# Kernel optimization log

Measured on AMD Instinct MI355X. Metric: run time of the kernel, lower is better.

The kernel has to match this reference:

```python
import jax, jax.numpy as jnp
import numpy as np

DIM = 256          # args.dim
MAX_Z = 100        # args.max_z
N_ATOM_EMBED = DIM - 1  # Euclidean manifold: dim - 1
B, N = 256, 128    # graphs, nodes per graph
E = B * N * N      # fully connected edges per batch, flattened
NORM_CONSTANT = 1.0


def setup_inputs() -> dict:
    key = jax.random.key(0)
    ks = jax.random.split(key, 8)
    x = jax.random.normal(ks[0], (B, N, 3), dtype=jnp.float32)
    categories = jax.random.randint(ks[1], (B, N), 0, MAX_Z)
    charges = jax.random.normal(ks[2], (B, N, 1), dtype=jnp.float32)
    edges = jax.random.randint(ks[3], (2, E), 0, B * N)
    node_mask = jnp.ones((B, N, 1), dtype=jnp.float32)
    edge_mask = jnp.ones((E, 1), dtype=jnp.float32)
    # nn.Embedding(max_z, n_atom_embed, padding_idx=0): row 0 is zeros
    emb = jax.random.normal(ks[4], (MAX_Z, N_ATOM_EMBED), dtype=jnp.float32)
    emb_table = emb.at[0].set(0.0)
    # nn.Linear(dim, 2*dim)
    lim = 1.0 / np.sqrt(DIM)
    W = jax.random.uniform(ks[5], (DIM, 2 * DIM), minval=-lim, maxval=lim, dtype=jnp.float32)
    b_lin = jax.random.uniform(ks[6], (2 * DIM,), minval=-lim, maxval=lim, dtype=jnp.float32)
    return {"x": x, "categories": categories, "charges": charges, "edges": edges,
            "node_mask": node_mask, "edge_mask": edge_mask,
            "emb_table": emb_table, "W": W, "b_lin": b_lin}


def coord2diff(x, edges, norm_constant=NORM_CONSTANT):
    row, col = edges[0], edges[1]
    coord_diff = x[row] - x[col]                              # [E, 3] gather + diff
    radial = jnp.sum(coord_diff * coord_diff, axis=1, keepdims=True)  # [E, 1]
    norm = jnp.sqrt(radial + 1e-8)
    coord_diff = coord_diff / (norm + norm_constant)
    return radial, coord_diff


def reference(x, categories, charges, edges, node_mask, edge_mask, emb_table, W, b_lin):
    h = emb_table[categories]                      # [B, N, dim-1] embedding lookup
    h = jnp.concatenate([charges, h], axis=2)      # [B, N, dim]
    b, n_nodes, d = h.shape
    xf = x.reshape(b * n_nodes, 3)
    nm = node_mask.reshape(b * n_nodes, 1)
    h = h.reshape(b * n_nodes, d) * nm             # masked node features
    radial, coord_diff = coord2diff(xf, edges)     # edge-index gather + norm
    # encode() pass-through (abstract layers treated as identity), then head
    parameters = h @ W + b_lin                     # [B*N, 2*dim] mean/logvar
    return parameters, radial, coord_diff
```

## Files before the change

### kernel.cpp

```cpp
#include <hip/hip_runtime.h>

typedef unsigned short u16;
typedef unsigned int u32;
typedef __attribute__((ext_vector_type(8))) short bf16x8;
typedef __attribute__((ext_vector_type(4))) float f32x4;

#define DIM 256
#define NOUT 512
#define MROWS 32768
#define NNODE 32768
#define NEDGE (256*128*128)
#define PARAM_SZ (32768*512)

__device__ __forceinline__ u16 f2bf(float f) {
    u32 x = __float_as_uint(f);
    u32 r = (x + 0x7FFFu + ((x >> 16) & 1u)) >> 16;
    return (u16)r;
}
__device__ __forceinline__ float bf2f(u16 u) {
    union { u32 i; float f; } v; v.i = ((u32)u) << 16; return v.f;
}

__global__ __launch_bounds__(1024) void transpose_kernel(const float* __restrict__ W,
                                                         u16* __restrict__ Wt) {
    __shared__ u16 tile[32][33];
    int n0 = blockIdx.x * 32;
    int k0 = blockIdx.y * 32;
    int tx = threadIdx.x, ty = threadIdx.y;
    tile[ty][tx] = f2bf(W[(k0 + ty) * NOUT + n0 + tx]);
    __syncthreads();
    Wt[(n0 + ty) * DIM + k0 + tx] = tile[tx][ty];
}

__global__ __launch_bounds__(256) void pack_kernel(const float* __restrict__ x,
                                                   const float* __restrict__ emb,
                                                   float4* __restrict__ xp,
                                                   u16* __restrict__ embp) {
    int i = blockIdx.x * 256 + threadIdx.x;
    if (i < NNODE) {
        float4 v;
        v.x = x[i * 3 + 0]; v.y = x[i * 3 + 1]; v.z = x[i * 3 + 2]; v.w = 0.0f;
        xp[i] = v;
    }
    if (i < 100 * 256) {
        int col = i & 255;
        int row = i >> 8;
        embp[i] = (col == 0) ? (u16)0 : f2bf(emb[row * 255 + col - 1]);
    }
}

__global__ __launch_bounds__(256) void edge_kernel(const int* __restrict__ edges,
                                                   const float4* __restrict__ xp,
                                                   float* __restrict__ radial_out,
                                                   float* __restrict__ cd_out) {
    __shared__ float buf[3072];
    const int tid = threadIdx.x;
    const int t4 = blockIdx.x * 256 + tid;
    int4 r4 = ((const int4*)edges)[t4];
    int4 c4 = ((const int4*)(edges + NEDGE))[t4];

    float4 xr0 = xp[r4.x], xr1 = xp[r4.y], xr2 = xp[r4.z], xr3 = xp[r4.w];
    float4 xc0 = xp[c4.x], xc1 = xp[c4.y], xc2 = xp[c4.z], xc3 = xp[c4.w];

    float4 rad;
    float cdv[12];
    #pragma unroll
    for (int e = 0; e < 4; ++e) {
        float4 a = (e == 0) ? xr0 : (e == 1) ? xr1 : (e == 2) ? xr2 : xr3;
        float4 b = (e == 0) ? xc0 : (e == 1) ? xc1 : (e == 2) ? xc2 : xc3;
        float dx = a.x - b.x, dy = a.y - b.y, dz = a.z - b.z;
        float r = dx * dx + dy * dy + dz * dz;
        float inv = 1.0f / (sqrtf(r + 1e-8f) + 1.0f);
        ((float*)&rad)[e] = r;
        cdv[e * 3 + 0] = dx * inv;
        cdv[e * 3 + 1] = dy * inv;
        cdv[e * 3 + 2] = dz * inv;
    }
    ((float4*)radial_out)[t4] = rad;

    #pragma unroll
    for (int k = 0; k < 3; ++k)
        ((float4*)buf)[tid * 3 + k] = ((const float4*)cdv)[k];
    __syncthreads();
    float4* cdg = (float4*)(cd_out + (size_t)blockIdx.x * 3072);
    #pragma unroll
    for (int k = 0; k < 3; ++k)
        cdg[k * 256 + tid] = ((const float4*)buf)[k * 256 + tid];
}

__global__ __launch_bounds__(256, 2) void gemm_kernel(const int* __restrict__ cats,
                                                      const float* __restrict__ charges,
                                                      const float* __restrict__ nmask,
                                                      const u16* __restrict__ embp,
                                                      const u16* __restrict__ Wt,
                                                      const float* __restrict__ bias,
                                                      float* __restrict__ out) {
    __shared__ u16 h_lds[64][DIM + 8];
    const int m0 = blockIdx.x * 64;
    const int tid = threadIdx.x;

    {
        int r = tid >> 2;
        int q = tid & 3;
        int m = m0 + r;
        float mask = nmask[m];
        const uint4* src = (const uint4*)(embp + (size_t)cats[m] * 256 + q * 64);
        uint4 v[8];
        #pragma unroll
        for (int t = 0; t < 8; ++t) v[t] = src[t];
        if (mask != 1.0f) {
            #pragma unroll
            for (int t = 0; t < 8; ++t) {
                u32* w = (u32*)&v[t];
                #pragma unroll
                for (int j = 0; j < 4; ++j) {
                    u16 lo = f2bf(bf2f((u16)(w[j] & 0xFFFF)) * mask);
                    u16 hi = f2bf(bf2f((u16)(w[j] >> 16)) * mask);
                    w[j] = (u32)lo | ((u32)hi << 16);
                }
            }
        }
        if (q == 0) {
            u32* w0 = (u32*)&v[0];
            w0[0] = (w0[0] & 0xFFFF0000u) | (u32)f2bf(charges[m] * mask);
        }
        #pragma unroll
        for (int t = 0; t < 8; ++t)
            *(uint4*)&h_lds[r][q * 64 + t * 8] = v[t];
    }
    __syncthreads();

    const int wave = tid >> 6;
    const int lane = tid & 63;
    const int lrow = lane & 15;
    const int quad = lane >> 4;
    const int nbase = wave * 128;

    f32x4 acc[4][8];
    #pragma unroll
    for (int ms = 0; ms < 4; ++ms)
        #pragma unroll
        for (int nt = 0; nt < 8; ++nt) acc[ms][nt] = (f32x4)(0.0f);

    #pragma unroll
    for (int k0 = 0; k0 < DIM; k0 += 32) {
        bf16x8 a[4];
        #pragma unroll
        for (int ms = 0; ms < 4; ++ms)
            a[ms] = *(const bf16x8*)&h_lds[ms * 16 + lrow][k0 + quad * 8];
        #pragma unroll
        for (int nt = 0; nt < 8; ++nt) {
            bf16x8 bfr = *(const bf16x8*)&Wt[(size_t)(nbase + nt * 16 + lrow) * DIM + k0 + quad * 8];
            #pragma unroll
            for (int ms = 0; ms < 4; ++ms)
                acc[ms][nt] = __builtin_amdgcn_mfma_f32_16x16x32_bf16(a[ms], bfr, acc[ms][nt], 0, 0, 0);
        }
    }

    #pragma unroll
    for (int nt = 0; nt < 8; ++nt) {
        int n = nbase + nt * 16 + lrow;
        float bv = bias[n];
        #pragma unroll
        for (int ms = 0; ms < 4; ++ms)
            #pragma unroll
            for (int r = 0; r < 4; ++r)
                out[(size_t)(m0 + ms * 16 + quad * 4 + r) * NOUT + n] = acc[ms][nt][r] + bv;
    }
}

extern "C" void kernel_launch(void* const* d_in, const int* in_sizes, int n_in,
                              void* d_out, int out_size, void* d_ws, size_t ws_size,
                              hipStream_t stream) {
    const float* x       = (const float*)d_in[0];
    const int*   cats    = (const int*)d_in[1];
    const float* charges = (const float*)d_in[2];
    const int*   edges   = (const int*)d_in[3];
    const float* nmask   = (const float*)d_in[4];
    const float* emb     = (const float*)d_in[6];
    const float* W       = (const float*)d_in[7];
    const float* bias    = (const float*)d_in[8];

    float* out    = (float*)d_out;
    float* params = out;
    float* radial = out + PARAM_SZ;
    float* cd     = out + PARAM_SZ + NEDGE;

    u16*    Wt   = (u16*)d_ws;
    float4* xp   = (float4*)((char*)d_ws + 256 * 1024);
    u16*    embp = (u16*)((char*)d_ws + 768 * 1024);

    transpose_kernel<<<dim3(16, 8), dim3(32, 32), 0, stream>>>(W, Wt);
    pack_kernel<<<NNODE / 256, 256, 0, stream>>>(x, emb, xp, embp);
    edge_kernel<<<NEDGE / 1024, 256, 0, stream>>>(edges, xp, radial, cd);
    gemm_kernel<<<MROWS / 64, 256, 0, stream>>>(cats, charges, nmask, embp, Wt, bias, params);
}
```

Measured before the change: 242.3 us.

## Merge prep kernels and co-schedule GEMM with edge work in one launch

Folds the weight transpose, coordinate packing and embedding packing into one prep kernel, cutting launches from four to two. The edge and GEMM kernels become one grid where the first 512 blocks do the GEMM and the remaining blocks do edges, so compute-bound and memory-bound work can share the GPU. In exchange, edge blocks now get the larger shared-memory footprint and the 256,2 launch bounds of the GEMM, which may lower their occupancy.

```diff
diff --git a/kernel.cpp b/kernel.cpp
--- a/kernel.cpp
+++ b/kernel.cpp
@@ -11,6 +11,8 @@
 #define NNODE 32768
 #define NEDGE (256*128*128)
 #define PARAM_SZ (32768*512)
+#define GEMM_BLOCKS 512
+#define EDGE_BLOCKS 4096
 
 __device__ __forceinline__ u16 f2bf(float f) {
     u32 x = __float_as_uint(f);
@@ -21,41 +23,51 @@
     union { u32 i; float f; } v; v.i = ((u32)u) << 16; return v.f;
 }
 
-__global__ __launch_bounds__(1024) void transpose_kernel(const float* __restrict__ W,
-                                                         u16* __restrict__ Wt) {
-    __shared__ u16 tile[32][33];
-    int n0 = blockIdx.x * 32;
-    int k0 = blockIdx.y * 32;
-    int tx = threadIdx.x, ty = threadIdx.y;
-    tile[ty][tx] = f2bf(W[(k0 + ty) * NOUT + n0 + tx]);
-    __syncthreads();
-    Wt[(n0 + ty) * DIM + k0 + tx] = tile[tx][ty];
-}
-
-__global__ __launch_bounds__(256) void pack_kernel(const float* __restrict__ x,
+__global__ __launch_bounds__(256) void prep_kernel(const float* __restrict__ W,
+                                                   const float* __restrict__ x,
                                                    const float* __restrict__ emb,
+                                                   u16* __restrict__ Wt,
                                                    float4* __restrict__ xp,
                                                    u16* __restrict__ embp) {
-    int i = blockIdx.x * 256 + threadIdx.x;
-    if (i < NNODE) {
+    const int b = blockIdx.x;
+    const int tid = threadIdx.x;
+    if (b < 128) {
+        __shared__ u16 tile[32][33];
+        int k0 = (b >> 4) * 32;
+        int n0 = (b & 15) * 32;
+        int tx = tid & 31, ty0 = tid >> 5;
+        #pragma unroll
+        for (int j = 0; j < 4; ++j) {
+            int ty = ty0 + j * 8;
+            tile[ty][tx] = f2bf(W[(k0 + ty) * NOUT + n0 + tx]);
+        }
+        __syncthreads();
+        #pragma unroll
+        for (int j = 0; j < 4; ++j) {
+            int ty = ty0 + j * 8;
+            Wt[(n0 + ty) * DIM + k0 + tx] = tile[tx][ty];
+        }
+    } else if (b < 256) {
+        int i = (b - 128) * 256 + tid;
         float4 v;
         v.x = x[i * 3 + 0]; v.y = x[i * 3 + 1]; v.z = x[i * 3 + 2]; v.w = 0.0f;
         xp[i] = v;
-    }
-    if (i < 100 * 256) {
+    } else {
+        int i = (b - 256) * 256 + tid;
         int col = i & 255;
         int row = i >> 8;
         embp[i] = (col == 0) ? (u16)0 : f2bf(emb[row * 255 + col - 1]);
     }
 }
 
-__global__ __launch_bounds__(256) void edge_kernel(const int* __restrict__ edges,
-                                                   const float4* __restrict__ xp,
-                                                   float* __restrict__ radial_out,
-                                                   float* __restrict__ cd_out) {
-    __shared__ float buf[3072];
-    const int tid = threadIdx.x;
-    const int t4 = blockIdx.x * 256 + tid;
+
+__device__ __forceinline__ void edge_part(int eb, int tid,
+                                          const int* __restrict__ edges,
+                                          const float4* __restrict__ xp,
+                                          float* __restrict__ radial_out,
+                                          float* __restrict__ cd_out,
+                                          float* buf ) {
+    const int t4 = eb * 256 + tid;
     int4 r4 = ((const int4*)edges)[t4];
     int4 c4 = ((const int4*)(edges + NEDGE))[t4];
 
@@ -82,22 +94,22 @@
     for (int k = 0; k < 3; ++k)
         ((float4*)buf)[tid * 3 + k] = ((const float4*)cdv)[k];
     __syncthreads();
-    float4* cdg = (float4*)(cd_out + (size_t)blockIdx.x * 3072);
+    float4* cdg = (float4*)(cd_out + (size_t)eb * 3072);
     #pragma unroll
     for (int k = 0; k < 3; ++k)
         cdg[k * 256 + tid] = ((const float4*)buf)[k * 256 + tid];
 }
 
-__global__ __launch_bounds__(256, 2) void gemm_kernel(const int* __restrict__ cats,
-                                                      const float* __restrict__ charges,
-                                                      const float* __restrict__ nmask,
-                                                      const u16* __restrict__ embp,
-                                                      const u16* __restrict__ Wt,
-                                                      const float* __restrict__ bias,
-                                                      float* __restrict__ out) {
-    __shared__ u16 h_lds[64][DIM + 8];
-    const int m0 = blockIdx.x * 64;
-    const int tid = threadIdx.x;
+__device__ __forceinline__ void gemm_part(int gb, int tid,
+                                          const int* __restrict__ cats,
+                                          const float* __restrict__ charges,
+                                          const float* __restrict__ nmask,
+                                          const u16* __restrict__ embp,
+                                          const u16* __restrict__ Wt,
+                                          const float* __restrict__ bias,
+                                          float* __restrict__ out,
+                                          u16 (*h_lds)[DIM + 8]) {
+    const int m0 = gb * 64;
 
     {
         int r = tid >> 2;
@@ -169,6 +181,26 @@
     }
 }
 
+__global__ __launch_bounds__(256, 2) void main_kernel(const int* __restrict__ cats,
+                                                      const float* __restrict__ charges,
+                                                      const float* __restrict__ nmask,
+                                                      const u16* __restrict__ embp,
+                                                      const u16* __restrict__ Wt,
+                                                      const float* __restrict__ bias,
+                                                      const int* __restrict__ edges,
+                                                      const float4* __restrict__ xp,
+                                                      float* __restrict__ params,
+                                                      float* __restrict__ radial,
+                                                      float* __restrict__ cd) {
+    __shared__ char smem[64 * (DIM + 8) * sizeof(u16)];
+    if (blockIdx.x < GEMM_BLOCKS)
+        gemm_part(blockIdx.x, threadIdx.x, cats, charges, nmask, embp, Wt, bias, params,
+                  (u16 (*)[DIM + 8])smem);
+    else
+        edge_part(blockIdx.x - GEMM_BLOCKS, threadIdx.x, edges, xp, radial, cd,
+                  (float*)smem);
+}
+
 extern "C" void kernel_launch(void* const* d_in, const int* in_sizes, int n_in,
                               void* d_out, int out_size, void* d_ws, size_t ws_size,
                               hipStream_t stream) {
@@ -190,8 +222,7 @@
     float4* xp   = (float4*)((char*)d_ws + 256 * 1024);
     u16*    embp = (u16*)((char*)d_ws + 768 * 1024);
 
-    transpose_kernel<<<dim3(16, 8), dim3(32, 32), 0, stream>>>(W, Wt);
-    pack_kernel<<<NNODE / 256, 256, 0, stream>>>(x, emb, xp, embp);
-    edge_kernel<<<NEDGE / 1024, 256, 0, stream>>>(edges, xp, radial, cd);
-    gemm_kernel<<<MROWS / 64, 256, 0, stream>>>(cats, charges, nmask, embp, Wt, bias, params);
-}
+    prep_kernel<<<356, 256, 0, stream>>>(W, x, emb, Wt, xp, embp);
+    main_kernel<<<GEMM_BLOCKS + EDGE_BLOCKS, 256, 0, stream>>>(
+        cats, charges, nmask, embp, Wt, bias, edges, xp, params, radial, cd);
+}
```

Result: faster. 233.0 us (-3.8%).
